# Kernel optimization log

Hardware: AMD Instinct MI355X
Metric: run time of the kernel (lower is better)

Reference implementation:

```python
import jax, jax.numpy as jnp
import numpy as np

D_MODEL = 512
N_HEADS = 8
MAX_DEPTH = 4
D_FF = 4 * D_MODEL
B, L = 4, 2048


def setup_inputs() -> dict:
    key = jax.random.key(0)
    ks = jax.random.split(key, 16)
    s = 0.02
    inp = {
        "x": jax.random.normal(ks[0], (B, L, D_MODEL), dtype=jnp.float32),
        # attention pre-norm
        "ln1_g": jnp.ones((D_MODEL,), jnp.float32),
        "ln1_b": jnp.zeros((D_MODEL,), jnp.float32),
        # MultiheadAttention in_proj (3D, D) and out_proj (D, D), torch (out, in) layout
        "Wqkv": jax.random.normal(ks[1], (3 * D_MODEL, D_MODEL), jnp.float32) * s,
        "bqkv": jnp.zeros((3 * D_MODEL,), jnp.float32),
        "Wo": jax.random.normal(ks[2], (D_MODEL, D_MODEL), jnp.float32) * s,
        "bo": jnp.zeros((D_MODEL,), jnp.float32),
        # FFN pre-norm + MLP
        "ln2_g": jnp.ones((D_MODEL,), jnp.float32),
        "ln2_b": jnp.zeros((D_MODEL,), jnp.float32),
        "W1": jax.random.normal(ks[3], (D_FF, D_MODEL), jnp.float32) * s,
        "b1": jnp.zeros((D_FF,), jnp.float32),
        "W2": jax.random.normal(ks[4], (D_MODEL, D_FF), jnp.float32) * s,
        "b2": jnp.zeros((D_MODEL,), jnp.float32),
        # token-choice depth router: LayerNorm + Linear(D,D) + GELU + Linear(D,max_depth)
        "rn_g": jnp.ones((D_MODEL,), jnp.float32),
        "rn_b": jnp.zeros((D_MODEL,), jnp.float32),
        "Rw1": jax.random.normal(ks[5], (D_MODEL, D_MODEL), jnp.float32) * s,
        "Rb1": jnp.zeros((D_MODEL,), jnp.float32),
        "Rw2": jax.random.normal(ks[6], (MAX_DEPTH, D_MODEL), jnp.float32) * s,
        "Rb2": jnp.zeros((MAX_DEPTH,), jnp.float32),
    }
    return inp


def _layernorm(x, g, b, eps=1e-5):
    mu = jnp.mean(x, axis=-1, keepdims=True)
    var = jnp.var(x, axis=-1, keepdims=True)
    return (x - mu) * jax.lax.rsqrt(var + eps) * g + b


def _block(x, ln1_g, ln1_b, Wqkv, bqkv, Wo, bo, ln2_g, ln2_b, W1, b1, W2, b2):
    Bb, Ll, D = x.shape
    H = N_HEADS
    dh = D // H
    # pre-norm self-attention
    h = _layernorm(x, ln1_g, ln1_b)
    qkv = h @ Wqkv.T + bqkv                      # (B, L, 3D)
    q, k, v = jnp.split(qkv, 3, axis=-1)
    q = q.reshape(Bb, Ll, H, dh)
    k = k.reshape(Bb, Ll, H, dh)
    v = v.reshape(Bb, Ll, H, dh)
    scores = jnp.einsum("blhd,bmhd->bhlm", q, k) / jnp.sqrt(jnp.float32(dh))
    attn = jax.nn.softmax(scores, axis=-1)
    o = jnp.einsum("bhlm,bmhd->blhd", attn, v).reshape(Bb, Ll, D)
    x = x + (o @ Wo.T + bo)
    # pre-norm FFN (exact-erf GELU, matching torch nn.GELU default)
    h2 = _layernorm(x, ln2_g, ln2_b)
    f = jax.nn.gelu(h2 @ W1.T + b1, approximate=False) @ W2.T + b2
    return x + f


def reference(x, ln1_g, ln1_b, Wqkv, bqkv, Wo, bo, ln2_g, ln2_b, W1, b1, W2, b2,
              rn_g, rn_b, Rw1, Rb1, Rw2, Rb2):
    # --- token-choice depth router (eval mode: argmax) ---
    rh = _layernorm(x, rn_g, rn_b)
    rh = jax.nn.gelu(rh @ Rw1.T + Rb1, approximate=False)
    router_logits = rh @ Rw2.T + Rb2             # (B, L, MAX_DEPTH)
    depths = jnp.argmax(router_logits, axis=-1) + 1  # (B, L) in [1, MAX_DEPTH]
    # --- dense recursion with torch.where-style selection ---
    cur = x
    for level in range(1, MAX_DEPTH + 1):
        upd = _block(cur, ln1_g, ln1_b, Wqkv, bqkv, Wo, bo,
                     ln2_g, ln2_b, W1, b1, W2, b2)
        keep = (depths >= level)[..., None]      # (B, L, 1)
        cur = jnp.where(keep, upd, cur)
    return cur, depths, router_logits
```

## Files before the change

### kernel.cpp

```cpp
#include <hip/hip_runtime.h>

typedef unsigned short u16;
typedef __attribute__((ext_vector_type(8))) short short8;
typedef __attribute__((ext_vector_type(4))) short s16x4;
typedef __attribute__((ext_vector_type(4))) float floatx4;
typedef __attribute__((ext_vector_type(4))) unsigned short u16x4;

#define NTOK 8192
#define DMODEL 512
#define DFF 2048
#define LSEQ 2048

__device__ __forceinline__ u16 f2bf(float f) {
    union { float f; unsigned u; } x; x.f = f;
    unsigned r = (x.u + 0x7fffu + ((x.u >> 16) & 1u)) >> 16;
    return (u16)r;
}

__device__ __forceinline__ float geluf(float x) {
    return 0.5f * x * (1.0f + erff(x * 0.70710678118654752f));
}

__device__ __forceinline__ void gload_lds16(const void* g, void* l) {
    __builtin_amdgcn_global_load_lds(
        (const __attribute__((address_space(1))) void*)g,
        (__attribute__((address_space(3))) void*)l,
        16, 0, 0);
}

__device__ __forceinline__ s16x4 pack_p(float p0, float p1, float p2, float p3) {
    union { float f; unsigned u; } a{p0}, b{p1}, c{p2}, d{p3};
    union { unsigned u[2]; s16x4 s; } r;
    r.u[0] = (a.u >> 16) | (b.u & 0xffff0000u);
    r.u[1] = (c.u >> 16) | (d.u & 0xffff0000u);
    return r.s;
}

__global__ __launch_bounds__(256) void cvt_w(const float* __restrict__ wq,
                                             const float* __restrict__ wo,
                                             const float* __restrict__ w1,
                                             const float* __restrict__ w2,
                                             u16* __restrict__ out) {
    int i = blockIdx.x * 256 + threadIdx.x;
    float v;
    if (i < 786432)       v = wq[i];
    else if (i < 1048576) v = wo[i - 786432];
    else if (i < 2097152) v = w1[i - 1048576];
    else                  v = w2[i - 2097152];
    out[i] = f2bf(v);
}

__global__ __launch_bounds__(256) void copy_f32(const float* __restrict__ a,
                                                float* __restrict__ b) {
    size_t i = ((size_t)blockIdx.x * 256 + threadIdx.x) * 4;
    *(floatx4*)&b[i] = *(const floatx4*)&a[i];
}

template<bool OUTF32>
__global__ __launch_bounds__(256)
void ln_k(const float* __restrict__ x, const float* __restrict__ g,
          const float* __restrict__ bb, void* __restrict__ outp) {
    const int row = blockIdx.x * 4 + (threadIdx.x >> 6);
    const int lane = threadIdx.x & 63;
    const float* xr = x + (size_t)row * DMODEL;
    const int c0 = lane * 4, c1 = c0 + 256;
    floatx4 a = *(const floatx4*)&xr[c0];
    floatx4 b = *(const floatx4*)&xr[c1];
    float s = 0.f, sq = 0.f;
#pragma unroll
    for (int e = 0; e < 4; ++e) { s += a[e]; sq += a[e] * a[e]; }
#pragma unroll
    for (int e = 0; e < 4; ++e) { s += b[e]; sq += b[e] * b[e]; }
#pragma unroll
    for (int m = 32; m >= 1; m >>= 1) {
        s += __shfl_xor(s, m);
        sq += __shfl_xor(sq, m);
    }
    const float mean = s * (1.f / 512.f);
    const float rstd = rsqrtf(sq * (1.f / 512.f) - mean * mean + 1e-5f);
    floatx4 g0 = *(const floatx4*)&g[c0];
    floatx4 g1 = *(const floatx4*)&g[c1];
    floatx4 b0 = *(const floatx4*)&bb[c0];
    floatx4 b1 = *(const floatx4*)&bb[c1];
    floatx4 y0, y1;
#pragma unroll
    for (int e = 0; e < 4; ++e) {
        y0[e] = (a[e] - mean) * rstd * g0[e] + b0[e];
        y1[e] = (b[e] - mean) * rstd * g1[e] + b1[e];
    }
    if (OUTF32) {
        float* o = (float*)outp + (size_t)row * DMODEL;
        *(floatx4*)&o[c0] = y0;
        *(floatx4*)&o[c1] = y1;
    } else {
        u16* o = (u16*)outp + (size_t)row * DMODEL;
        u16x4 p0, p1;
#pragma unroll
        for (int e = 0; e < 4; ++e) { p0[e] = f2bf(y0[e]); p1[e] = f2bf(y1[e]); }
        *(u16x4*)&o[c0] = p0;
        *(u16x4*)&o[c1] = p1;
    }
}

template<int EPI, int BN>
__global__ __launch_bounds__(256, 2)
void gemm_bt(const u16* __restrict__ A, const u16* __restrict__ Bw,
             const float* __restrict__ bias,
             u16* __restrict__ Cb, float* __restrict__ Cf,
             const float* __restrict__ res, const float* __restrict__ depth,
             float aux, int N, int K) {
    constexpr int NJ = BN / 32;
    __shared__ __align__(16) u16 As[128 * 32];
    __shared__ __align__(16) u16 Bs[BN * 32];
    const int tid = threadIdx.x;
    const int lane = tid & 63;
    const int w = tid >> 6;
    const int wm = (w >> 1) * 64;
    const int wn = (w & 1) * (BN / 2);
    const int mBase = blockIdx.x * 128;
    const int nBase = blockIdx.y * BN;
    const int q4 = lane >> 4, rl = lane & 15;

    floatx4 acc[4][NJ];
#pragma unroll
    for (int i = 0; i < 4; ++i)
#pragma unroll
        for (int j = 0; j < NJ; ++j) acc[i][j] = (floatx4){0.f, 0.f, 0.f, 0.f};

    const int i0 = tid, i1 = tid + 256;
    const int ar0 = i0 >> 2, ac0 = ((i0 & 3) ^ ((i0 >> 3) & 3)) * 8;
    const int ar1 = i1 >> 2, ac1 = ((i1 & 3) ^ ((i1 >> 3) & 3)) * 8;
    const u16* pA0 = A + (size_t)(mBase + ar0) * K + ac0;
    const u16* pA1 = A + (size_t)(mBase + ar1) * K + ac1;
    const u16* pB0 = Bw + (size_t)(nBase + ar0) * K + ac0;
    const u16* pB1 = (BN == 128) ? Bw + (size_t)(nBase + ar1) * K + ac1 : pB0;
    u16* lA0 = &As[i0 * 8];
    u16* lA1 = &As[i1 * 8];
    u16* lB0 = &Bs[i0 * 8];
    u16* lB1 = (BN == 128) ? &Bs[i1 * 8] : lB0;

    for (int k0 = 0; k0 < K; k0 += 32) {
        gload_lds16(pA0, lA0);
        gload_lds16(pA1, lA1);
        gload_lds16(pB0, lB0);
        if (BN == 128) gload_lds16(pB1, lB1);
        pA0 += 32; pA1 += 32; pB0 += 32;
        if (BN == 128) pB1 += 32;
        __syncthreads();
        short8 af[4], bf[NJ];
#pragma unroll
        for (int t = 0; t < 4; ++t) {
            const int r = wm + t * 16 + rl;
            af[t] = *(const short8*)&As[r * 32 + (q4 ^ ((r >> 1) & 3)) * 8];
        }
#pragma unroll
        for (int t = 0; t < NJ; ++t) {
            const int r = wn + t * 16 + rl;
            bf[t] = *(const short8*)&Bs[r * 32 + (q4 ^ ((r >> 1) & 3)) * 8];
        }
#pragma unroll
        for (int ti = 0; ti < 4; ++ti)
#pragma unroll
            for (int tj = 0; tj < NJ; ++tj)
                acc[ti][tj] = __builtin_amdgcn_mfma_f32_16x16x32_bf16(
                    af[ti], bf[tj], acc[ti][tj], 0, 0, 0);
        __syncthreads();
    }

#pragma unroll
    for (int ti = 0; ti < 4; ++ti) {
        const int r0 = mBase + wm + ti * 16 + q4 * 4;
#pragma unroll
        for (int tj = 0; tj < NJ; ++tj) {
            const int c = nBase + wn + tj * 16 + rl;
            const float bv = bias[c];
#pragma unroll
            for (int rr = 0; rr < 4; ++rr) {
                const int r = r0 + rr;
                float v = acc[ti][tj][rr] + bv;
                if (EPI == 0) {
                    if (c < 512) v *= aux;
                    Cb[(size_t)r * N + c] = f2bf(v);
                } else if (EPI == 1) {
                    Cb[(size_t)r * N + c] = f2bf(geluf(v));
                } else if (EPI == 2) {
                    Cf[(size_t)r * N + c] = res[(size_t)r * N + c] + v;
                } else {
                    if (depth[r] >= aux)
                        Cf[(size_t)r * N + c] = res[(size_t)r * N + c] + v;
                }
            }
        }
    }
}

__global__ __launch_bounds__(256, 2)
void attn_k(const u16* __restrict__ qkv, u16* __restrict__ o) {
    const int qt = blockIdx.x;
    const int bh = blockIdx.y;
    const int b = bh >> 3, h = bh & 7;
    const int tid = threadIdx.x, lane = tid & 63, w = tid >> 6;
    const int tok0 = b * LSEQ;
    const int qrow0 = qt * 128 + w * 32;
    const int q4 = lane >> 4, rl = lane & 15;

    __shared__ __align__(16) u16 Kt[128 * 64];
    __shared__ __align__(16) u16 Vt[64 * 132];

    short8 qf[2][2];
#pragma unroll
    for (int nt = 0; nt < 2; ++nt)
#pragma unroll
        for (int ks = 0; ks < 2; ++ks)
            qf[nt][ks] = *(const short8*)&qkv[(size_t)(tok0 + qrow0 + nt * 16 + rl) * 1536
                                              + h * 64 + ks * 32 + q4 * 8];

    floatx4 oacc[4][2];
#pragma unroll
    for (int dt = 0; dt < 4; ++dt)
#pragma unroll
        for (int nt = 0; nt < 2; ++nt) oacc[dt][nt] = (floatx4){0.f, 0.f, 0.f, 0.f};
    float lsum[2] = {0.f, 0.f};

    for (int kt = 0; kt < 16; ++kt) {
        const int kv0 = kt * 128;
        __syncthreads();
#pragma unroll
        for (int it = 0; it < 4; ++it) {
            const int i = it * 256 + tid;
            const int r = i >> 3;
            const int c = ((i & 7) ^ (r & 7)) * 8;
            gload_lds16(&qkv[(size_t)(tok0 + kv0 + r) * 1536 + 512 + h * 64 + c],
                        &Kt[i * 8]);
        }
        {
            const int c = tid & 63;
            const int r0 = (tid >> 6) * 4;
#pragma unroll
            for (int it = 0; it < 8; ++it) {
                const int r = r0 + it * 16;
                const u16* vp = &qkv[(size_t)(tok0 + kv0 + r) * 1536 + 1024 + h * 64 + c];
                u16x4 pk;
                pk[0] = vp[0]; pk[1] = vp[1536]; pk[2] = vp[3072]; pk[3] = vp[4608];
                *(u16x4*)&Vt[c * 132 + r] = pk;
            }
        }
        __syncthreads();

#pragma unroll
        for (int mt = 0; mt < 8; ++mt) {
            const int r = mt * 16 + rl;
            short8 kf0 = *(const short8*)&Kt[r * 64 + ((q4) ^ (r & 7)) * 8];
            short8 kf1 = *(const short8*)&Kt[r * 64 + ((4 + q4) ^ (r & 7)) * 8];
            floatx4 s[2];
#pragma unroll
            for (int nt = 0; nt < 2; ++nt) {
                s[nt] = __builtin_amdgcn_mfma_f32_16x16x32_bf16(kf0, qf[nt][0],
                        (floatx4){0.f, 0.f, 0.f, 0.f}, 0, 0, 0);
                s[nt] = __builtin_amdgcn_mfma_f32_16x16x32_bf16(kf1, qf[nt][1],
                        s[nt], 0, 0, 0);
            }
            s16x4 pb[2];
#pragma unroll
            for (int nt = 0; nt < 2; ++nt) {
                const float p0 = exp2f(s[nt][0]);
                const float p1 = exp2f(s[nt][1]);
                const float p2 = exp2f(s[nt][2]);
                const float p3 = exp2f(s[nt][3]);
                lsum[nt] += (p0 + p1) + (p2 + p3);
                pb[nt] = pack_p(p0, p1, p2, p3);
            }
#pragma unroll
            for (int dt = 0; dt < 4; ++dt) {
                s16x4 vf = *(const s16x4*)&Vt[(dt * 16 + rl) * 132 + mt * 16 + q4 * 4];
#pragma unroll
                for (int nt = 0; nt < 2; ++nt)
                    oacc[dt][nt] = __builtin_amdgcn_mfma_f32_16x16x16bf16_1k(
                        vf, pb[nt], oacc[dt][nt], 0, 0, 0);
            }
        }
    }

#pragma unroll
    for (int nt = 0; nt < 2; ++nt) {
        float l = lsum[nt];
        l += __shfl_xor(l, 16);
        l += __shfl_xor(l, 32);
        const float inv = 1.0f / l;
        const size_t row = tok0 + qrow0 + nt * 16 + rl;
#pragma unroll
        for (int dt = 0; dt < 4; ++dt) {
            u16x4 pk;
#pragma unroll
            for (int rr = 0; rr < 4; ++rr) pk[rr] = f2bf(oacc[dt][nt][rr] * inv);
            *(u16x4*)&o[row * DMODEL + h * 64 + dt * 16 + q4 * 4] = pk;
        }
    }
}

__global__ __launch_bounds__(256, 2)
void router_gemm1(const float* __restrict__ A, const float* __restrict__ W,
                  const float* __restrict__ bias, float* __restrict__ out) {
    __shared__ float Af[32][68];
    __shared__ float Bf[32][132];
    const int tid = threadIdx.x;
    const int tx = tid & 15, ty = tid >> 4;
    const int mb = blockIdx.x * 64, nb = blockIdx.y * 128;
    double acc[4][8] = {};
    for (int k0 = 0; k0 < 512; k0 += 32) {
#pragma unroll
        for (int it = 0; it < 2; ++it) {
            const int ch = tid + it * 256;
            const int m = ch >> 3, c4 = (ch & 7) * 4;
            const floatx4 v = *(const floatx4*)&A[(size_t)(mb + m) * 512 + k0 + c4];
#pragma unroll
            for (int e = 0; e < 4; ++e) Af[c4 + e][m] = v[e];
        }
#pragma unroll
        for (int it = 0; it < 4; ++it) {
            const int ch = tid + it * 256;
            const int n = ch >> 3, c4 = (ch & 7) * 4;
            const floatx4 v = *(const floatx4*)&W[(size_t)(nb + n) * 512 + k0 + c4];
#pragma unroll
            for (int e = 0; e < 4; ++e) Bf[c4 + e][n] = v[e];
        }
        __syncthreads();
#pragma unroll 4
        for (int kk = 0; kk < 32; ++kk) {
            const floatx4 a4 = *(const floatx4*)&Af[kk][ty * 4];
            double av[4], bv[8];
#pragma unroll
            for (int i = 0; i < 4; ++i) av[i] = (double)a4[i];
#pragma unroll
            for (int j = 0; j < 8; ++j) bv[j] = (double)Bf[kk][tx + 16 * j];
#pragma unroll
            for (int i = 0; i < 4; ++i)
#pragma unroll
                for (int j = 0; j < 8; ++j)
                    acc[i][j] = fma(av[i], bv[j], acc[i][j]);
        }
        __syncthreads();
    }
#pragma unroll
    for (int i = 0; i < 4; ++i) {
        const int r = mb + ty * 4 + i;
#pragma unroll
        for (int j = 0; j < 8; ++j) {
            const int c = nb + tx + 16 * j;
            out[(size_t)r * 512 + c] = geluf((float)(acc[i][j] + (double)bias[c]));
        }
    }
}

__global__ __launch_bounds__(256)
void router_logits_k(const float* __restrict__ rr, const float* __restrict__ Rw2,
                     const float* __restrict__ Rb2, float* __restrict__ logits,
                     float* __restrict__ depthf) {
    const int t = blockIdx.x * 4 + (threadIdx.x >> 6);
    const int lane = threadIdx.x & 63;
    const float* xr = rr + (size_t)t * 512;
    const int c0 = lane * 4, c1 = c0 + 256;
    floatx4 a = *(const floatx4*)&xr[c0];
    floatx4 b = *(const floatx4*)&xr[c1];
    double s[4];
#pragma unroll
    for (int d = 0; d < 4; ++d) {
        const float* wr = Rw2 + d * 512;
        floatx4 wa = *(const floatx4*)&wr[c0];
        floatx4 wb = *(const floatx4*)&wr[c1];
        double acc = 0.0;
#pragma unroll
        for (int e = 0; e < 4; ++e) acc += (double)a[e] * (double)wa[e];
#pragma unroll
        for (int e = 0; e < 4; ++e) acc += (double)b[e] * (double)wb[e];
        s[d] = acc;
    }
#pragma unroll
    for (int m = 32; m >= 1; m >>= 1)
#pragma unroll
        for (int d = 0; d < 4; ++d) s[d] += __shfl_xor(s[d], m);
    if (lane == 0) {
        double bv = -1e300;
        int best = 0;
#pragma unroll
        for (int d = 0; d < 4; ++d) {
            const double v = s[d] + (double)Rb2[d];
            logits[(size_t)t * 4 + d] = (float)v;
            if (v > bv) { bv = v; best = d; }
        }
        depthf[t] = (float)(best + 1);
    }
}

extern "C" void kernel_launch(void* const* d_in, const int* in_sizes, int n_in,
                              void* d_out, int out_size, void* d_ws, size_t ws_size,
                              hipStream_t stream) {
    (void)in_sizes; (void)n_in; (void)out_size; (void)ws_size;
    const float* x    = (const float*)d_in[0];
    const float* ln1g = (const float*)d_in[1];
    const float* ln1b = (const float*)d_in[2];
    const float* Wqkv = (const float*)d_in[3];
    const float* bqkv = (const float*)d_in[4];
    const float* Wo   = (const float*)d_in[5];
    const float* bo   = (const float*)d_in[6];
    const float* ln2g = (const float*)d_in[7];
    const float* ln2b = (const float*)d_in[8];
    const float* W1   = (const float*)d_in[9];
    const float* b1   = (const float*)d_in[10];
    const float* W2   = (const float*)d_in[11];
    const float* b2   = (const float*)d_in[12];
    const float* rng  = (const float*)d_in[13];
    const float* rnb  = (const float*)d_in[14];
    const float* Rw1  = (const float*)d_in[15];
    const float* Rb1  = (const float*)d_in[16];
    const float* Rw2  = (const float*)d_in[17];
    const float* Rb2  = (const float*)d_in[18];

    float* cur    = (float*)d_out;
    float* depthf = cur + (size_t)NTOK * DMODEL;
    float* logits = depthf + NTOK;

    char* ws = (char*)d_ws;
    float* xmid = (float*)ws;
    u16* sbuf   = (u16*)(ws + 16777216);
    u16* qkvb   = (u16*)(ws + 25165824);
    u16* ffb    = (u16*)(ws + 50331648);
    u16* wbf    = (u16*)(ws + 83886080);
    float* rrf  = (float*)ffb;

    u16* wq = wbf;
    u16* wo = wbf + 786432;
    u16* w1 = wbf + 1048576;
    u16* w2 = wbf + 2097152;

    const float qsc = 0.125f * 1.4426950408889634f;

    cvt_w<<<12288, 256, 0, stream>>>(Wqkv, Wo, W1, W2, wbf);
    copy_f32<<<4096, 256, 0, stream>>>(x, cur);

    ln_k<true><<<2048, 256, 0, stream>>>(x, rng, rnb, xmid);
    router_gemm1<<<dim3(128, 4), 256, 0, stream>>>(xmid, Rw1, Rb1, rrf);
    router_logits_k<<<2048, 256, 0, stream>>>(rrf, Rw2, Rb2, logits, depthf);

    for (int level = 1; level <= 4; ++level) {
        ln_k<false><<<2048, 256, 0, stream>>>(cur, ln1g, ln1b, sbuf);
        gemm_bt<0, 128><<<dim3(64, 12), 256, 0, stream>>>(
            sbuf, wq, bqkv, qkvb, nullptr, nullptr, nullptr, qsc, 1536, 512);
        attn_k<<<dim3(16, 32), 256, 0, stream>>>(qkvb, sbuf);
        gemm_bt<2, 64><<<dim3(64, 8), 256, 0, stream>>>(
            sbuf, wo, bo, nullptr, xmid, cur, nullptr, 0.f, 512, 512);
        ln_k<false><<<2048, 256, 0, stream>>>(xmid, ln2g, ln2b, sbuf);
        gemm_bt<1, 128><<<dim3(64, 16), 256, 0, stream>>>(
            sbuf, w1, b1, ffb, nullptr, nullptr, nullptr, 0.f, 2048, 512);
        gemm_bt<3, 64><<<dim3(64, 8), 256, 0, stream>>>(
            ffb, w2, b2, nullptr, cur, xmid, depthf, (float)level, 512, 2048);
    }
}
```

Before: 1.046 ms.

## Write V transposed from QKV GEMM and halve attention query tile

The QKV GEMM epilogue now writes Q and K into a 1024-wide buffer and V directly in a per-head transposed layout (head, dh, kv). The attention kernel can then load V into LDS with async global-to-LDS copies using an XOR swizzle, instead of doing scalar strided loads and manual transposition. The attention kernel also processes 64 query rows per block (16 per wave) with launch bounds of 4 blocks per CU, doubling grid size to raise occupancy. The tradeoff is less K/V reuse per block and scattered 8-byte stores in the GEMM epilogue for V.

```diff
diff --git a/kernel.cpp b/kernel.cpp
--- a/kernel.cpp
+++ b/kernel.cpp
@@ -108,6 +108,7 @@
              const float* __restrict__ bias,
              u16* __restrict__ Cb, float* __restrict__ Cf,
              const float* __restrict__ res, const float* __restrict__ depth,
+             u16* __restrict__ Cv,
              float aux, int N, int K) {
     constexpr int NJ = BN / 32;
     __shared__ __align__(16) u16 As[128 * 32];
@@ -174,53 +175,68 @@
         for (int tj = 0; tj < NJ; ++tj) {
             const int c = nBase + wn + tj * 16 + rl;
             const float bv = bias[c];
-#pragma unroll
-            for (int rr = 0; rr < 4; ++rr) {
-                const int r = r0 + rr;
-                float v = acc[ti][tj][rr] + bv;
-                if (EPI == 0) {
-                    if (c < 512) v *= aux;
-                    Cb[(size_t)r * N + c] = f2bf(v);
-                } else if (EPI == 1) {
-                    Cb[(size_t)r * N + c] = f2bf(geluf(v));
-                } else if (EPI == 2) {
-                    Cf[(size_t)r * N + c] = res[(size_t)r * N + c] + v;
+            if (EPI == 0) {
+                if (nBase < 1024) {
+                    const float sc = (nBase < 512) ? aux : 1.0f;
+#pragma unroll
+                    for (int rr = 0; rr < 4; ++rr)
+                        Cb[(size_t)(r0 + rr) * 1024 + c] =
+                            f2bf((acc[ti][tj][rr] + bv) * sc);
                 } else {
-                    if (depth[r] >= aux)
+                    const int cm = c - 1024;
+                    const int hh = cm >> 6, dh = cm & 63;
+                    const int bb2 = r0 >> 11, kv = r0 & 2047;
+                    u16x4 pk;
+#pragma unroll
+                    for (int rr = 0; rr < 4; ++rr)
+                        pk[rr] = f2bf(acc[ti][tj][rr] + bv);
+                    *(u16x4*)&Cv[((size_t)(bb2 * 8 + hh) * 64 + dh) * 2048 + kv] = pk;
+                }
+            } else {
+#pragma unroll
+                for (int rr = 0; rr < 4; ++rr) {
+                    const int r = r0 + rr;
+                    const float v = acc[ti][tj][rr] + bv;
+                    if (EPI == 1) {
+                        Cb[(size_t)r * N + c] = f2bf(geluf(v));
+                    } else if (EPI == 2) {
                         Cf[(size_t)r * N + c] = res[(size_t)r * N + c] + v;
+                    } else {
+                        if (depth[r] >= aux)
+                            Cf[(size_t)r * N + c] = res[(size_t)r * N + c] + v;
+                    }
                 }
             }
         }
     }
 }
 
-__global__ __launch_bounds__(256, 2)
-void attn_k(const u16* __restrict__ qkv, u16* __restrict__ o) {
+__global__ __launch_bounds__(256, 4)
+void attn_k(const u16* __restrict__ qk, const u16* __restrict__ vT,
+            u16* __restrict__ o) {
     const int qt = blockIdx.x;
     const int bh = blockIdx.y;
     const int b = bh >> 3, h = bh & 7;
     const int tid = threadIdx.x, lane = tid & 63, w = tid >> 6;
     const int tok0 = b * LSEQ;
-    const int qrow0 = qt * 128 + w * 32;
+    const int qrow0 = qt * 64 + w * 16;
     const int q4 = lane >> 4, rl = lane & 15;
 
     __shared__ __align__(16) u16 Kt[128 * 64];
-    __shared__ __align__(16) u16 Vt[64 * 132];
-
-    short8 qf[2][2];
-#pragma unroll
-    for (int nt = 0; nt < 2; ++nt)
-#pragma unroll
-        for (int ks = 0; ks < 2; ++ks)
-            qf[nt][ks] = *(const short8*)&qkv[(size_t)(tok0 + qrow0 + nt * 16 + rl) * 1536
-                                              + h * 64 + ks * 32 + q4 * 8];
-
-    floatx4 oacc[4][2];
-#pragma unroll
-    for (int dt = 0; dt < 4; ++dt)
-#pragma unroll
-        for (int nt = 0; nt < 2; ++nt) oacc[dt][nt] = (floatx4){0.f, 0.f, 0.f, 0.f};
-    float lsum[2] = {0.f, 0.f};
+    __shared__ __align__(16) u16 Vt[64 * 128];
+
+    const u16* vbase = vT + (size_t)bh * 64 * 2048;
+
+    short8 qf[2];
+#pragma unroll
+    for (int ks = 0; ks < 2; ++ks)
+        qf[ks] = *(const short8*)&qk[(size_t)(tok0 + qrow0 + rl) * 1024
+                                      + h * 64 + ks * 32 + q4 * 8];
+
+    floatx4 oacc[4];
+#pragma unroll
+    for (int dt = 0; dt < 4; ++dt) oacc[dt] = (floatx4){0.f, 0.f, 0.f, 0.f};
+    float lsum = 0.f;
 
     for (int kt = 0; kt < 16; ++kt) {
         const int kv0 = kt * 128;
@@ -230,20 +246,15 @@
             const int i = it * 256 + tid;
             const int r = i >> 3;
             const int c = ((i & 7) ^ (r & 7)) * 8;
-            gload_lds16(&qkv[(size_t)(tok0 + kv0 + r) * 1536 + 512 + h * 64 + c],
+            gload_lds16(&qk[(size_t)(tok0 + kv0 + r) * 1024 + 512 + h * 64 + c],
                         &Kt[i * 8]);
         }
-        {
-            const int c = tid & 63;
-            const int r0 = (tid >> 6) * 4;
-#pragma unroll
-            for (int it = 0; it < 8; ++it) {
-                const int r = r0 + it * 16;
-                const u16* vp = &qkv[(size_t)(tok0 + kv0 + r) * 1536 + 1024 + h * 64 + c];
-                u16x4 pk;
-                pk[0] = vp[0]; pk[1] = vp[1536]; pk[2] = vp[3072]; pk[3] = vp[4608];
-                *(u16x4*)&Vt[c * 132 + r] = pk;
-            }
+#pragma unroll
+        for (int it = 0; it < 4; ++it) {
+            const int i = it * 256 + tid;
+            const int dh = i >> 4;
+            const int ch = (i & 15) ^ (dh & 15);
+            gload_lds16(&vbase[(size_t)dh * 2048 + kv0 + ch * 8], &Vt[i * 8]);
         }
         __syncthreads();
 
@@ -252,49 +263,38 @@
             const int r = mt * 16 + rl;
             short8 kf0 = *(const short8*)&Kt[r * 64 + ((q4) ^ (r & 7)) * 8];
             short8 kf1 = *(const short8*)&Kt[r * 64 + ((4 + q4) ^ (r & 7)) * 8];
-            floatx4 s[2];
-#pragma unroll
-            for (int nt = 0; nt < 2; ++nt) {
-                s[nt] = __builtin_amdgcn_mfma_f32_16x16x32_bf16(kf0, qf[nt][0],
-                        (floatx4){0.f, 0.f, 0.f, 0.f}, 0, 0, 0);
-                s[nt] = __builtin_amdgcn_mfma_f32_16x16x32_bf16(kf1, qf[nt][1],
-                        s[nt], 0, 0, 0);
+            floatx4 s;
+            s = __builtin_amdgcn_mfma_f32_16x16x32_bf16(kf0, qf[0],
+                    (floatx4){0.f, 0.f, 0.f, 0.f}, 0, 0, 0);
+            s = __builtin_amdgcn_mfma_f32_16x16x32_bf16(kf1, qf[1], s, 0, 0, 0);
+            const float p0 = exp2f(s[0]);
+            const float p1 = exp2f(s[1]);
+            const float p2 = exp2f(s[2]);
+            const float p3 = exp2f(s[3]);
+            lsum += (p0 + p1) + (p2 + p3);
+            const s16x4 pb = pack_p(p0, p1, p2, p3);
+            const int ct = 2 * mt + (q4 >> 1);
+#pragma unroll
+            for (int dt = 0; dt < 4; ++dt) {
+                const s16x4 vf = *(const s16x4*)&Vt[(dt * 16 + rl) * 128
+                                                    + (ct ^ rl) * 8 + (q4 & 1) * 4];
+                oacc[dt] = __builtin_amdgcn_mfma_f32_16x16x16bf16_1k(
+                    vf, pb, oacc[dt], 0, 0, 0);
             }
-            s16x4 pb[2];
-#pragma unroll
-            for (int nt = 0; nt < 2; ++nt) {
-                const float p0 = exp2f(s[nt][0]);
-                const float p1 = exp2f(s[nt][1]);
-                const float p2 = exp2f(s[nt][2]);
-                const float p3 = exp2f(s[nt][3]);
-                lsum[nt] += (p0 + p1) + (p2 + p3);
-                pb[nt] = pack_p(p0, p1, p2, p3);
-            }
-#pragma unroll
-            for (int dt = 0; dt < 4; ++dt) {
-                s16x4 vf = *(const s16x4*)&Vt[(dt * 16 + rl) * 132 + mt * 16 + q4 * 4];
-#pragma unroll
-                for (int nt = 0; nt < 2; ++nt)
-                    oacc[dt][nt] = __builtin_amdgcn_mfma_f32_16x16x16bf16_1k(
-                        vf, pb[nt], oacc[dt][nt], 0, 0, 0);
-            }
-        }
-    }
-
-#pragma unroll
-    for (int nt = 0; nt < 2; ++nt) {
-        float l = lsum[nt];
-        l += __shfl_xor(l, 16);
-        l += __shfl_xor(l, 32);
-        const float inv = 1.0f / l;
-        const size_t row = tok0 + qrow0 + nt * 16 + rl;
-#pragma unroll
-        for (int dt = 0; dt < 4; ++dt) {
-            u16x4 pk;
-#pragma unroll
-            for (int rr = 0; rr < 4; ++rr) pk[rr] = f2bf(oacc[dt][nt][rr] * inv);
-            *(u16x4*)&o[row * DMODEL + h * 64 + dt * 16 + q4 * 4] = pk;
-        }
+        }
+    }
+
+    float l = lsum;
+    l += __shfl_xor(l, 16);
+    l += __shfl_xor(l, 32);
+    const float inv = 1.0f / l;
+    const size_t row = tok0 + qrow0 + rl;
+#pragma unroll
+    for (int dt = 0; dt < 4; ++dt) {
+        u16x4 pk;
+#pragma unroll
+        for (int rr = 0; rr < 4; ++rr) pk[rr] = f2bf(oacc[dt][rr] * inv);
+        *(u16x4*)&o[row * DMODEL + h * 64 + dt * 16 + q4 * 4] = pk;
     }
 }
 
@@ -423,8 +423,9 @@
     char* ws = (char*)d_ws;
     float* xmid = (float*)ws;
     u16* sbuf   = (u16*)(ws + 16777216);
-    u16* qkvb   = (u16*)(ws + 25165824);
-    u16* ffb    = (u16*)(ws + 50331648);
+    u16* qk     = (u16*)(ws + 25165824);
+    u16* ffb    = (u16*)(ws + 41943040);
+    u16* vTb    = (u16*)(ws + 75497472);
     u16* wbf    = (u16*)(ws + 83886080);
     float* rrf  = (float*)ffb;
 
@@ -445,14 +446,14 @@
     for (int level = 1; level <= 4; ++level) {
         ln_k<false><<<2048, 256, 0, stream>>>(cur, ln1g, ln1b, sbuf);
         gemm_bt<0, 128><<<dim3(64, 12), 256, 0, stream>>>(
-            sbuf, wq, bqkv, qkvb, nullptr, nullptr, nullptr, qsc, 1536, 512);
-        attn_k<<<dim3(16, 32), 256, 0, stream>>>(qkvb, sbuf);
+            sbuf, wq, bqkv, qk, nullptr, nullptr, nullptr, vTb, qsc, 1536, 512);
+        attn_k<<<dim3(32, 32), 256, 0, stream>>>(qk, vTb, sbuf);
         gemm_bt<2, 64><<<dim3(64, 8), 256, 0, stream>>>(
-            sbuf, wo, bo, nullptr, xmid, cur, nullptr, 0.f, 512, 512);
+            sbuf, wo, bo, nullptr, xmid, cur, nullptr, nullptr, 0.f, 512, 512);
         ln_k<false><<<2048, 256, 0, stream>>>(xmid, ln2g, ln2b, sbuf);
         gemm_bt<1, 128><<<dim3(64, 16), 256, 0, stream>>>(
-            sbuf, w1, b1, ffb, nullptr, nullptr, nullptr, 0.f, 2048, 512);
+            sbuf, w1, b1, ffb, nullptr, nullptr, nullptr, nullptr, 0.f, 2048, 512);
         gemm_bt<3, 64><<<dim3(64, 8), 256, 0, stream>>>(
-            ffb, w2, b2, nullptr, cur, xmid, depthf, (float)level, 512, 2048);
-    }
-}
+            ffb, w2, b2, nullptr, cur, xmid, depthf, nullptr, (float)level, 512, 2048);
+    }
+}
```

After: 941.0 us. 1.11x faster.
